# Performance work log

Measured on AMD Instinct MI355X. Metric: run time of the kernel, lower is better.

## Reference

```python
import jax, jax.numpy as jnp
import numpy as np
import math

B, T, EMB, HEAD = 4, 4096, 768, 64


def setup_inputs() -> dict:
    key = jax.random.key(0)
    kx, kk, kq, kv = jax.random.split(key, 4)
    s = 1.0 / math.sqrt(EMB)  # roughly torch Linear init scale
    return {
        "x": jax.random.normal(kx, (B, T, EMB), dtype=jnp.float32),
        "Wk": jax.random.normal(kk, (EMB, HEAD), dtype=jnp.float32) * s,
        "Wq": jax.random.normal(kq, (EMB, HEAD), dtype=jnp.float32) * s,
        "Wv": jax.random.normal(kv, (EMB, HEAD), dtype=jnp.float32) * s,
    }


def reference(x, Wk, Wq, Wv):
    # x: (B, T, EMB); projections are bias-free Linear layers
    k = x @ Wk  # (B, T, HEAD)
    q = x @ Wq
    v = x @ Wv
    Tcur = x.shape[1]
    scale = 1.0 / math.sqrt(k.shape[-1])
    # (B, Tq, Tk) score matrix, causal masked
    wei = jnp.einsum("bqh,bkh->bqk", q, k) * scale
    causal = jnp.tril(jnp.ones((Tcur, Tcur), dtype=bool))
    wei = jnp.where(causal, wei, -jnp.inf)
    attn = jax.nn.softmax(wei, axis=-1)  # dropout p=0.0 (eval)
    return jnp.einsum("bqk,bkh->bqh", attn, v)  # (B, T, HEAD)
```

## Files before the change

### kernel.cpp

```cpp
#include <hip/hip_runtime.h>
#include <hip/hip_bf16.h>

#define NB 4
#define NT 4096
#define NE 768
#define NH 64

using bf16 = __hip_bfloat16;
typedef __attribute__((ext_vector_type(8))) short bf16x8;
typedef __attribute__((ext_vector_type(4))) float f32x4;
typedef __attribute__((ext_vector_type(16))) float f32x16;
typedef __attribute__((ext_vector_type(4))) unsigned int u32x4;

#define QSCALE 0.18033688011112042f

__device__ inline short f2bfs(float f) {
  bf16 h = __float2bfloat16(f);
  return __builtin_bit_cast(short, h);
}
__device__ inline unsigned pack_bf2(float a, float b) {
  unsigned short ua = __builtin_bit_cast(unsigned short, __float2bfloat16(a));
  unsigned short ub = __builtin_bit_cast(unsigned short, __float2bfloat16(b));
  return ((unsigned)ub << 16) | ua;
}

#define GLOAD_LDS16(gsrc, ldst)                                        \
  __builtin_amdgcn_global_load_lds(                                    \
      (const __attribute__((address_space(1))) void*)(gsrc),           \
      (__attribute__((address_space(3))) void*)(ldst), 16, 0, 0)

__global__ __launch_bounds__(256) void k_wt(const float* __restrict__ Wk,
                                            const float* __restrict__ Wq,
                                            const float* __restrict__ Wv,
                                            bf16* __restrict__ Wt2) {
  __shared__ float xl[32][65];
  const int m = blockIdx.x / 24;
  const int ks = blockIdx.x % 24;
  const int tid = threadIdx.x;
  const float* W = (m == 0) ? Wk : ((m == 1) ? Wq : Wv);
  const float scale = (m == 1) ? QSCALE : 1.0f;
  const int e0 = ks * 32;
#pragma unroll
  for (int i = 0; i < 8; ++i) {
    const int lin = i * 256 + tid;
    xl[lin >> 6][lin & 63] = W[(size_t)(e0 + (lin >> 6)) * NH + (lin & 63)];
  }
  __syncthreads();
  const int lane = tid & 63, w = tid >> 6;
  const int cbg = m * 4 + w;
  bf16x8 t;
#pragma unroll
  for (int j = 0; j < 8; ++j)
    t[j] = f2bfs(xl[((lane >> 4) << 3) + j][w * 16 + (lane & 15)] * scale);
  *reinterpret_cast<bf16x8*>(Wt2 + (((size_t)cbg * 24 + ks) * 64 + lane) * 8) = t;
}

__global__ __launch_bounds__(256) void k_proj(const float* __restrict__ x,
                                              const bf16* __restrict__ Wt2,
                                              bf16* __restrict__ Q,
                                              bf16* __restrict__ K,
                                              bf16* __restrict__ Vt) {
  __shared__ __align__(16) bf16 xl[16][768];
  const int tid = threadIdx.x;
  const int wave = tid >> 6, lane = tid & 63;
  const int lr = lane & 15, lk = lane >> 4;
  const int row0 = blockIdx.x * 16;

#pragma unroll
  for (int j = 0; j < 6; ++j) {
    const int e = (j * 256 + tid) * 8;
    const int row = e / 768;
    const int col = e - row * 768;
    const int chunk = col >> 3;
    const int sch = (chunk & ~7) | ((chunk ^ row) & 7);
    const float* xp = x + (size_t)(row0 + row) * NE + col;
    float4 a0 = *reinterpret_cast<const float4*>(xp);
    float4 a1 = *reinterpret_cast<const float4*>(xp + 4);
    bf16x8 af;
    af[0] = f2bfs(a0.x); af[1] = f2bfs(a0.y); af[2] = f2bfs(a0.z); af[3] = f2bfs(a0.w);
    af[4] = f2bfs(a1.x); af[5] = f2bfs(a1.y); af[6] = f2bfs(a1.z); af[7] = f2bfs(a1.w);
    *reinterpret_cast<bf16x8*>((char*)xl + row * 1536 + sch * 16) = af;
  }
  __syncthreads();

  f32x4 acc[3];
#pragma unroll
  for (int cb = 0; cb < 3; ++cb)
#pragma unroll
    for (int r = 0; r < 4; ++r) acc[cb][r] = 0.f;

#pragma unroll 4
  for (int ks = 0; ks < 24; ++ks) {
    const int chunk = ks * 4 + lk;
    const int sch = (chunk & ~7) | ((chunk ^ lr) & 7);
    bf16x8 af = *reinterpret_cast<const bf16x8*>((const char*)xl + lr * 1536 + sch * 16);
#pragma unroll
    for (int cb = 0; cb < 3; ++cb) {
      bf16x8 bfr = *reinterpret_cast<const bf16x8*>(
          Wt2 + (((size_t)(wave * 3 + cb) * 24 + ks) * 64 + lane) * 8);
      acc[cb] = __builtin_amdgcn_mfma_f32_16x16x32_bf16(af, bfr, acc[cb], 0, 0, 0);
    }
  }

  const int trow = row0 + lk * 4;
#pragma unroll
  for (int cb = 0; cb < 3; ++cb) {
    const int hh0 = (wave * 3 + cb) * 16;
    const int m = hh0 >> 6;
    const int h = (hh0 & 63) + lr;
    if (m == 0) {
#pragma unroll
      for (int r = 0; r < 4; ++r)
        K[(size_t)(trow + r) * NH + h] = __float2bfloat16(acc[cb][r]);
    } else if (m == 1) {
#pragma unroll
      for (int r = 0; r < 4; ++r)
        Q[(size_t)(trow + r) * NH + h] = __float2bfloat16(acc[cb][r]);
    } else {
      const int bb = trow >> 12;
      const int t = trow & (NT - 1);
      ushort4 pk;
      pk.x = (unsigned short)f2bfs(acc[cb][0]);
      pk.y = (unsigned short)f2bfs(acc[cb][1]);
      pk.z = (unsigned short)f2bfs(acc[cb][2]);
      pk.w = (unsigned short)f2bfs(acc[cb][3]);
      *reinterpret_cast<ushort4*>(Vt + (size_t)(bb * NH + h) * NT + t) = pk;
    }
  }
}

__device__ inline void stage_kv(const bf16* Kb, const bf16* Vb, int k0,
                                bf16* Kl, bf16* Vl, int wave, int lane) {
  const int rsub = lane >> 3, ch = lane & 7;
#pragma unroll
  for (int j = 0; j < 2; ++j) {
    const int br = j * 32 + wave * 8;
    const int row = br + rsub;
    const int sch = ch ^ (row & 7);
    GLOAD_LDS16(Kb + (size_t)(k0 + row) * NH + sch * 8, Kl + br * 64);
    GLOAD_LDS16(Vb + (size_t)row * NT + k0 + sch * 8, Vl + br * 64);
  }
}

__global__ __launch_bounds__(256) void k_attn_part(const bf16* __restrict__ Q,
                                                   const bf16* __restrict__ K,
                                                   const bf16* __restrict__ Vt,
                                                   float* __restrict__ part_o,
                                                   float* __restrict__ part_ml,
                                                   int CH, int MAXC) {
  __shared__ __align__(16) bf16 Kl[2][64][64];
  __shared__ __align__(16) bf16 Vl[2][64][64];
  const int tid = threadIdx.x;
  const int wave = tid >> 6, lane = tid & 63;
  const int l31 = lane & 31, hi5 = lane >> 5;
  const int gid = blockIdx.x;
  const int c = gid % MAXC;
  const int srs = (gid / MAXC) & 31;
  const int b = gid / (MAXC * 32);
  const int s = 31 - srs;
  const int ntiles = 2 * s + 2;
  const int nch = (ntiles + CH - 1) / CH;
  if (c >= nch) return;
  const int kt0 = c * CH;
  const int kt1 = min(kt0 + CH, ntiles);
  const int qblk = s * 128;
  const int qrow = 8 * wave + (l31 & 7) + 32 * (l31 >> 3);
  const int qcol = qblk + qrow;

  const bf16* Qb = Q + (size_t)(b * NT + qcol) * NH;
  const bf16* Kb = K + (size_t)b * NT * NH;
  const bf16* Vb = Vt + (size_t)b * NH * NT;

  bf16x8 qf[4];
#pragma unroll
  for (int ks = 0; ks < 4; ++ks)
    qf[ks] = *reinterpret_cast<const bf16x8*>(Qb + ks * 16 + hi5 * 8);

  f32x16 o[2];
#pragma unroll
  for (int hb = 0; hb < 2; ++hb)
#pragma unroll
    for (int r = 0; r < 16; ++r) o[hb][r] = 0.f;
  float m = -1e30f, lsum = 0.f;

  stage_kv(Kb, Vb, kt0 * 64, &Kl[0][0][0], &Vl[0][0][0], wave, lane);

  for (int kt = kt0; kt < kt1; ++kt) {
    const int buf = (kt - kt0) & 1;
    __syncthreads();
    if (kt + 1 < kt1)
      stage_kv(Kb, Vb, (kt + 1) * 64, &Kl[buf ^ 1][0][0], &Vl[buf ^ 1][0][0], wave, lane);
    const int k0 = kt * 64;
    const bf16* Klb = &Kl[buf][0][0];
    const bf16* Vlb = &Vl[buf][0][0];

    f32x16 sa[2];
#pragma unroll
    for (int kb = 0; kb < 2; ++kb) {
#pragma unroll
      for (int r = 0; r < 16; ++r) sa[kb][r] = 0.f;
      __builtin_amdgcn_s_setprio(1);
#pragma unroll
      for (int ks = 0; ks < 4; ++ks) {
        const int row = l31 + 32 * kb;
        const int sch = (hi5 + 2 * ks) ^ (row & 7);
        bf16x8 kf = *reinterpret_cast<const bf16x8*>(Klb + row * 64 + sch * 8);
        sa[kb] = __builtin_amdgcn_mfma_f32_32x32x16_bf16(kf, qf[ks], sa[kb], 0, 0, 0);
      }
      __builtin_amdgcn_s_setprio(0);
    }
    if (kt >= 2 * s) {
#pragma unroll
      for (int kb = 0; kb < 2; ++kb)
#pragma unroll
        for (int r = 0; r < 16; ++r) {
          const int kg = k0 + (r & 3) + 8 * (r >> 2) + 4 * hi5 + 32 * kb;
          if (kg > qcol) sa[kb][r] = -1e30f;
        }
    }
    float pm = sa[0][0];
#pragma unroll
    for (int r = 1; r < 16; ++r) pm = fmaxf(pm, sa[0][r]);
#pragma unroll
    for (int r = 0; r < 16; ++r) pm = fmaxf(pm, sa[1][r]);
    pm = fmaxf(pm, __shfl_xor(pm, 32));
    if (!__all(pm - m <= 6.f)) {
      const float mn = fmaxf(m, pm);
      const float alpha = exp2f(m - mn);
      lsum *= alpha;
#pragma unroll
      for (int hb = 0; hb < 2; ++hb)
#pragma unroll
        for (int r = 0; r < 16; ++r) o[hb][r] *= alpha;
      m = mn;
    }
    float rs = 0.f;
#pragma unroll
    for (int kb = 0; kb < 2; ++kb)
#pragma unroll
      for (int r = 0; r < 16; ++r) {
        const float p = exp2f(sa[kb][r] - m);
        sa[kb][r] = p;
        rs += p;
      }
    rs += __shfl_xor(rs, 32);
    lsum += rs;
    unsigned pk[2][4][2];
#pragma unroll
    for (int kb = 0; kb < 2; ++kb)
#pragma unroll
      for (int q4 = 0; q4 < 4; ++q4)
#pragma unroll
        for (int p = 0; p < 2; ++p)
          pk[kb][q4][p] = pack_bf2(sa[kb][4 * q4 + 2 * p], sa[kb][4 * q4 + 2 * p + 1]);
#pragma unroll
    for (int kb16 = 0; kb16 < 4; ++kb16) {
      const int kb32 = kb16 >> 1;
      const int q4a = 2 * (kb16 & 1);
      const unsigned X0 = pk[kb32][q4a][0], X1 = pk[kb32][q4a][1];
      const unsigned Y0 = pk[kb32][q4a + 1][0], Y1 = pk[kb32][q4a + 1][1];
      const unsigned pX0 = __shfl_xor((int)X0, 32), pX1 = __shfl_xor((int)X1, 32);
      const unsigned pY0 = __shfl_xor((int)Y0, 32), pY1 = __shfl_xor((int)Y1, 32);
      u32x4 pw;
      pw[0] = hi5 ? pY0 : X0;
      pw[1] = hi5 ? pY1 : X1;
      pw[2] = hi5 ? Y0 : pX0;
      pw[3] = hi5 ? Y1 : pX1;
      const bf16x8 pf = __builtin_bit_cast(bf16x8, pw);
      __builtin_amdgcn_s_setprio(1);
#pragma unroll
      for (int hb = 0; hb < 2; ++hb) {
        const int row = l31 + 32 * hb;
        const int sch = (hi5 + 2 * kb16) ^ (row & 7);
        bf16x8 vf = *reinterpret_cast<const bf16x8*>(Vlb + row * 64 + sch * 8);
        o[hb] = __builtin_amdgcn_mfma_f32_32x32x16_bf16(vf, pf, o[hb], 0, 0, 0);
      }
      __builtin_amdgcn_s_setprio(0);
    }
  }

  const size_t idx = (size_t)(b * 32 + s) * MAXC + c;
  float* po = part_o + idx * (128 * 64);
#pragma unroll
  for (int hb = 0; hb < 2; ++hb)
#pragma unroll
    for (int q4 = 0; q4 < 4; ++q4) {
      const int h0 = 32 * hb + 8 * q4 + 4 * hi5;
      float4 v;
      v.x = o[hb][4 * q4 + 0];
      v.y = o[hb][4 * q4 + 1];
      v.z = o[hb][4 * q4 + 2];
      v.w = o[hb][4 * q4 + 3];
      *reinterpret_cast<float4*>(po + (size_t)qrow * 64 + h0) = v;
    }
  if (hi5 == 0) {
    float* pml = part_ml + idx * 256;
    pml[qrow] = m;
    pml[128 + qrow] = lsum;
  }
}

__global__ __launch_bounds__(256) void k_attn_comb(const float* __restrict__ part_o,
                                                   const float* __restrict__ part_ml,
                                                   float* __restrict__ out,
                                                   int CH, int MAXC) {
  const int gid = blockIdx.x;
  const int s = gid & 31;
  const int b = gid >> 5;
  const int row = threadIdx.x >> 1;
  const int half = threadIdx.x & 1;
  const int ntiles = 2 * s + 2;
  const int nc = (ntiles + CH - 1) / CH;
  const size_t base = (size_t)(b * 32 + s) * MAXC;

  float M = -1e30f;
  for (int c = 0; c < nc; ++c)
    M = fmaxf(M, part_ml[(base + c) * 256 + row]);
  float L = 0.f;
  float4 a[8];
#pragma unroll
  for (int k = 0; k < 8; ++k) a[k] = float4{0, 0, 0, 0};
  for (int c = 0; c < nc; ++c) {
    const float mc = part_ml[(base + c) * 256 + row];
    const float lc = part_ml[(base + c) * 256 + 128 + row];
    const float sc = exp2f(mc - M);
    L += lc * sc;
    const float4* op = reinterpret_cast<const float4*>(
        part_o + (base + c) * (128 * 64) + (size_t)row * 64 + half * 32);
#pragma unroll
    for (int k = 0; k < 8; ++k) {
      const float4 v = op[k];
      a[k].x += v.x * sc; a[k].y += v.y * sc;
      a[k].z += v.z * sc; a[k].w += v.w * sc;
    }
  }
  const float inv = 1.f / L;
  float4* outp = reinterpret_cast<float4*>(
      out + (size_t)(b * NT + s * 128 + row) * NH + half * 32);
#pragma unroll
  for (int k = 0; k < 8; ++k) {
    a[k].x *= inv; a[k].y *= inv; a[k].z *= inv; a[k].w *= inv;
    outp[k] = a[k];
  }
}

extern "C" void kernel_launch(void* const* d_in, const int* in_sizes, int n_in,
                              void* d_out, int out_size, void* d_ws, size_t ws_size,
                              hipStream_t stream) {
  const float* x  = (const float*)d_in[0];
  const float* Wk = (const float*)d_in[1];
  const float* Wq = (const float*)d_in[2];
  const float* Wv = (const float*)d_in[3];
  float* out = (float*)d_out;

  char* ws = (char*)d_ws;
  const size_t sz_wt  = (size_t)3 * NH * NE * sizeof(bf16);
  const size_t sz_qkv = (size_t)NB * NT * NH * sizeof(bf16);
  const size_t off_q  = (sz_wt + 255) & ~size_t(255);
  const size_t off_k  = off_q + sz_qkv;
  const size_t off_vt = off_k + sz_qkv;
  const size_t off_pp = off_vt + sz_qkv;

  const size_t per_chunk = (size_t)(128 * 64 + 256) * sizeof(float);
  int CH = 64, MAXC = 1;
  const int opts_ch[3]   = {6, 8, 16};
  const int opts_maxc[3] = {11, 8, 4};
  for (int i = 0; i < 3; ++i) {
    const size_t need = off_pp + (size_t)NB * 32 * opts_maxc[i] * per_chunk;
    if (ws_size >= need) { CH = opts_ch[i]; MAXC = opts_maxc[i]; break; }
  }
  const size_t n_idx = (size_t)NB * 32 * MAXC;
  const size_t off_po = off_pp;
  const size_t off_ml = off_po + n_idx * (128 * 64) * sizeof(float);

  bf16* Wt2 = (bf16*)(ws);
  bf16* Qw  = (bf16*)(ws + off_q);
  bf16* Kw  = (bf16*)(ws + off_k);
  bf16* Vtw = (bf16*)(ws + off_vt);
  float* part_o  = (float*)(ws + off_po);
  float* part_ml = (float*)(ws + off_ml);

  hipLaunchKernelGGL(k_wt, dim3(3 * 24), dim3(256), 0, stream, Wk, Wq, Wv, Wt2);
  hipLaunchKernelGGL(k_proj, dim3(NB * NT / 16), dim3(256), 0, stream,
                     x, Wt2, Qw, Kw, Vtw);
  hipLaunchKernelGGL(k_attn_part, dim3(NB * 32 * MAXC), dim3(256), 0, stream,
                     Qw, Kw, Vtw, part_o, part_ml, CH, MAXC);
  hipLaunchKernelGGL(k_attn_comb, dim3(NB * 32), dim3(256), 0, stream,
                     part_o, part_ml, out, CH, MAXC);
}
```

Baseline: 157.3 us.

## Software-pipeline QK^T ahead of softmax/PV, bf16 partials, wider projection and combine

The attention split kernel now triple-buffers K and double-buffers V, computing the next tile's QK^T scores before the current tile's softmax and PV MFMAs so that matrix work overlaps the exp/reduction phase. Partial outputs are stored as bf16 instead of fp32, which halves partial-buffer traffic but adds rounding error before the combine. The projection kernel processes 32 rows per block, reusing each weight fragment for two MFMAs. The combine kernel launches eight times more blocks, each handling fewer columns per thread. Register pressure rises from the extra score accumulators held across the pipeline.

```diff
diff --git a/kernel.cpp b/kernel.cpp
--- a/kernel.cpp
+++ b/kernel.cpp
@@ -17,6 +17,10 @@
 __device__ inline short f2bfs(float f) {
   bf16 h = __float2bfloat16(f);
   return __builtin_bit_cast(short, h);
+}
+__device__ inline float bfs2f(unsigned short u) {
+  unsigned v = ((unsigned)u) << 16;
+  return __builtin_bit_cast(float, v);
 }
 __device__ inline unsigned pack_bf2(float a, float b) {
   unsigned short ua = __builtin_bit_cast(unsigned short, __float2bfloat16(a));
@@ -60,14 +64,14 @@
                                               bf16* __restrict__ Q,
                                               bf16* __restrict__ K,
                                               bf16* __restrict__ Vt) {
-  __shared__ __align__(16) bf16 xl[16][768];
+  __shared__ __align__(16) bf16 xl[32][768];
   const int tid = threadIdx.x;
   const int wave = tid >> 6, lane = tid & 63;
   const int lr = lane & 15, lk = lane >> 4;
-  const int row0 = blockIdx.x * 16;
-
-#pragma unroll
-  for (int j = 0; j < 6; ++j) {
+  const int row0 = blockIdx.x * 32;
+
+#pragma unroll
+  for (int j = 0; j < 12; ++j) {
     const int e = (j * 256 + tid) * 8;
     const int row = e / 768;
     const int col = e - row * 768;
@@ -83,72 +87,182 @@
   }
   __syncthreads();
 
-  f32x4 acc[3];
+  f32x4 acc0[3], acc1[3];
 #pragma unroll
   for (int cb = 0; cb < 3; ++cb)
 #pragma unroll
-    for (int r = 0; r < 4; ++r) acc[cb][r] = 0.f;
+    for (int r = 0; r < 4; ++r) { acc0[cb][r] = 0.f; acc1[cb][r] = 0.f; }
 
 #pragma unroll 4
   for (int ks = 0; ks < 24; ++ks) {
     const int chunk = ks * 4 + lk;
     const int sch = (chunk & ~7) | ((chunk ^ lr) & 7);
-    bf16x8 af = *reinterpret_cast<const bf16x8*>((const char*)xl + lr * 1536 + sch * 16);
+    bf16x8 af0 = *reinterpret_cast<const bf16x8*>((const char*)xl + lr * 1536 + sch * 16);
+    bf16x8 af1 = *reinterpret_cast<const bf16x8*>((const char*)xl + (16 + lr) * 1536 + sch * 16);
 #pragma unroll
     for (int cb = 0; cb < 3; ++cb) {
       bf16x8 bfr = *reinterpret_cast<const bf16x8*>(
           Wt2 + (((size_t)(wave * 3 + cb) * 24 + ks) * 64 + lane) * 8);
-      acc[cb] = __builtin_amdgcn_mfma_f32_16x16x32_bf16(af, bfr, acc[cb], 0, 0, 0);
+      acc0[cb] = __builtin_amdgcn_mfma_f32_16x16x32_bf16(af0, bfr, acc0[cb], 0, 0, 0);
+      acc1[cb] = __builtin_amdgcn_mfma_f32_16x16x32_bf16(af1, bfr, acc1[cb], 0, 0, 0);
     }
   }
 
-  const int trow = row0 + lk * 4;
-#pragma unroll
-  for (int cb = 0; cb < 3; ++cb) {
-    const int hh0 = (wave * 3 + cb) * 16;
-    const int m = hh0 >> 6;
-    const int h = (hh0 & 63) + lr;
-    if (m == 0) {
-#pragma unroll
-      for (int r = 0; r < 4; ++r)
-        K[(size_t)(trow + r) * NH + h] = __float2bfloat16(acc[cb][r]);
-    } else if (m == 1) {
-#pragma unroll
-      for (int r = 0; r < 4; ++r)
-        Q[(size_t)(trow + r) * NH + h] = __float2bfloat16(acc[cb][r]);
-    } else {
-      const int bb = trow >> 12;
-      const int t = trow & (NT - 1);
-      ushort4 pk;
-      pk.x = (unsigned short)f2bfs(acc[cb][0]);
-      pk.y = (unsigned short)f2bfs(acc[cb][1]);
-      pk.z = (unsigned short)f2bfs(acc[cb][2]);
-      pk.w = (unsigned short)f2bfs(acc[cb][3]);
-      *reinterpret_cast<ushort4*>(Vt + (size_t)(bb * NH + h) * NT + t) = pk;
+#pragma unroll
+  for (int st = 0; st < 2; ++st) {
+    const int trow = row0 + st * 16 + lk * 4;
+#pragma unroll
+    for (int cb = 0; cb < 3; ++cb) {
+      const f32x4 a = st ? acc1[cb] : acc0[cb];
+      const int hh0 = (wave * 3 + cb) * 16;
+      const int m = hh0 >> 6;
+      const int h = (hh0 & 63) + lr;
+      if (m == 0) {
+#pragma unroll
+        for (int r = 0; r < 4; ++r)
+          K[(size_t)(trow + r) * NH + h] = __float2bfloat16(a[r]);
+      } else if (m == 1) {
+#pragma unroll
+        for (int r = 0; r < 4; ++r)
+          Q[(size_t)(trow + r) * NH + h] = __float2bfloat16(a[r]);
+      } else {
+        const int bb = trow >> 12;
+        const int t = trow & (NT - 1);
+        ushort4 pk;
+        pk.x = (unsigned short)f2bfs(a[0]);
+        pk.y = (unsigned short)f2bfs(a[1]);
+        pk.z = (unsigned short)f2bfs(a[2]);
+        pk.w = (unsigned short)f2bfs(a[3]);
+        *reinterpret_cast<ushort4*>(Vt + (size_t)(bb * NH + h) * NT + t) = pk;
+      }
     }
   }
 }
 
-__device__ inline void stage_kv(const bf16* Kb, const bf16* Vb, int k0,
-                                bf16* Kl, bf16* Vl, int wave, int lane) {
+__device__ inline void stage_k(const bf16* Kb, int k0, bf16* Kd, int wave, int lane) {
   const int rsub = lane >> 3, ch = lane & 7;
 #pragma unroll
   for (int j = 0; j < 2; ++j) {
     const int br = j * 32 + wave * 8;
     const int row = br + rsub;
     const int sch = ch ^ (row & 7);
-    GLOAD_LDS16(Kb + (size_t)(k0 + row) * NH + sch * 8, Kl + br * 64);
-    GLOAD_LDS16(Vb + (size_t)row * NT + k0 + sch * 8, Vl + br * 64);
-  }
-}
+    GLOAD_LDS16(Kb + (size_t)(k0 + row) * NH + sch * 8, Kd + br * 64);
+  }
+}
+__device__ inline void stage_v(const bf16* Vb, int k0, bf16* Vd, int wave, int lane) {
+  const int rsub = lane >> 3, ch = lane & 7;
+#pragma unroll
+  for (int j = 0; j < 2; ++j) {
+    const int br = j * 32 + wave * 8;
+    const int row = br + rsub;
+    const int sch = ch ^ (row & 7);
+    GLOAD_LDS16(Vb + (size_t)row * NT + k0 + sch * 8, Vd + br * 64);
+  }
+}
+
+#define QK_TILE(SA, KBUF, KT)                                                 \
+  {                                                                           \
+    const bf16* kbp_ = (KBUF);                                                \
+    _Pragma("unroll")                                                         \
+    for (int kb = 0; kb < 2; ++kb) {                                          \
+      _Pragma("unroll") for (int r = 0; r < 16; ++r) SA[kb][r] = 0.f;         \
+      __builtin_amdgcn_s_setprio(1);                                          \
+      _Pragma("unroll")                                                       \
+      for (int ks = 0; ks < 4; ++ks) {                                        \
+        const int row_ = l31 + 32 * kb;                                       \
+        const int sch_ = (hi5 + 2 * ks) ^ (row_ & 7);                         \
+        bf16x8 kf_ = *reinterpret_cast<const bf16x8*>(kbp_ + row_ * 64 + sch_ * 8); \
+        SA[kb] = __builtin_amdgcn_mfma_f32_32x32x16_bf16(kf_, qf[ks], SA[kb], 0, 0, 0); \
+      }                                                                       \
+      __builtin_amdgcn_s_setprio(0);                                          \
+    }                                                                         \
+    if ((KT) >= 2 * s) {                                                      \
+      _Pragma("unroll")                                                       \
+      for (int kb = 0; kb < 2; ++kb)                                          \
+        _Pragma("unroll") for (int r = 0; r < 16; ++r) {                      \
+          const int kg_ = (KT) * 64 + (r & 3) + 8 * (r >> 2) + 4 * hi5 + 32 * kb; \
+          if (kg_ > qcol) SA[kb][r] = -1e30f;                                 \
+        }                                                                     \
+    }                                                                         \
+  }
+
+#define TILE_BODY(SC, SN, I)                                                  \
+  {                                                                           \
+    __syncthreads();                                                          \
+    if ((I) + 2 < n) stage_k(Kb, (kt0 + (I) + 2) * 64, &Kl[((I) + 2) % 3][0][0], wave, lane); \
+    if ((I) + 1 < n) {                                                        \
+      stage_v(Vb, (kt0 + (I) + 1) * 64, &Vl[((I) + 1) & 1][0][0], wave, lane); \
+      QK_TILE(SN, &Kl[((I) + 1) % 3][0][0], kt0 + (I) + 1);                   \
+    }                                                                         \
+                               \
+    float t0_[8];                                                             \
+    _Pragma("unroll")                                                         \
+    for (int r = 0; r < 8; ++r)                                               \
+      t0_[r] = fmaxf(fmaxf(SC[0][r], SC[0][r + 8]), fmaxf(SC[1][r], SC[1][r + 8])); \
+    float pm = fmaxf(fmaxf(fmaxf(t0_[0], t0_[1]), fmaxf(t0_[2], t0_[3])),     \
+                     fmaxf(fmaxf(t0_[4], t0_[5]), fmaxf(t0_[6], t0_[7])));    \
+    pm = fmaxf(pm, __shfl_xor(pm, 32));                                       \
+    if (!__all(pm - m <= 6.f)) {                                              \
+      const float mn = fmaxf(m, pm);                                          \
+      const float alpha = exp2f(m - mn);                                      \
+      lsum *= alpha;                                                          \
+      _Pragma("unroll")                                                       \
+      for (int hb = 0; hb < 2; ++hb)                                          \
+        _Pragma("unroll") for (int r = 0; r < 16; ++r) o[hb][r] *= alpha;     \
+      m = mn;                                                                 \
+    }                                                                         \
+    float rs0 = 0.f, rs1 = 0.f, rs2 = 0.f, rs3 = 0.f;                         \
+    _Pragma("unroll")                                                         \
+    for (int kb = 0; kb < 2; ++kb)                                            \
+      _Pragma("unroll") for (int r = 0; r < 16; r += 4) {                     \
+        SC[kb][r] = exp2f(SC[kb][r] - m); rs0 += SC[kb][r];                   \
+        SC[kb][r + 1] = exp2f(SC[kb][r + 1] - m); rs1 += SC[kb][r + 1];       \
+        SC[kb][r + 2] = exp2f(SC[kb][r + 2] - m); rs2 += SC[kb][r + 2];       \
+        SC[kb][r + 3] = exp2f(SC[kb][r + 3] - m); rs3 += SC[kb][r + 3];       \
+      }                                                                       \
+    float rs = (rs0 + rs1) + (rs2 + rs3);                                     \
+    rs += __shfl_xor(rs, 32);                                                 \
+    lsum += rs;                                                               \
+    unsigned pk[2][4][2];                                                     \
+    _Pragma("unroll")                                                         \
+    for (int kb = 0; kb < 2; ++kb)                                            \
+      _Pragma("unroll") for (int q4 = 0; q4 < 4; ++q4)                        \
+        _Pragma("unroll") for (int p = 0; p < 2; ++p)                         \
+          pk[kb][q4][p] = pack_bf2(SC[kb][4 * q4 + 2 * p], SC[kb][4 * q4 + 2 * p + 1]); \
+    const bf16* Vlb_ = &Vl[(I) & 1][0][0];                                    \
+    _Pragma("unroll")                                                         \
+    for (int kb16 = 0; kb16 < 4; ++kb16) {                                    \
+      const int kb32 = kb16 >> 1;                                             \
+      const int q4a = 2 * (kb16 & 1);                                         \
+      const unsigned X0 = pk[kb32][q4a][0], X1 = pk[kb32][q4a][1];            \
+      const unsigned Y0 = pk[kb32][q4a + 1][0], Y1 = pk[kb32][q4a + 1][1];    \
+      const unsigned pX0 = __shfl_xor((int)X0, 32), pX1 = __shfl_xor((int)X1, 32); \
+      const unsigned pY0 = __shfl_xor((int)Y0, 32), pY1 = __shfl_xor((int)Y1, 32); \
+      u32x4 pw;                                                               \
+      pw[0] = hi5 ? pY0 : X0;                                                 \
+      pw[1] = hi5 ? pY1 : X1;                                                 \
+      pw[2] = hi5 ? Y0 : pX0;                                                 \
+      pw[3] = hi5 ? Y1 : pX1;                                                 \
+      const bf16x8 pf = __builtin_bit_cast(bf16x8, pw);                       \
+      __builtin_amdgcn_s_setprio(1);                                          \
+      _Pragma("unroll")                                                       \
+      for (int hb = 0; hb < 2; ++hb) {                                        \
+        const int row_ = l31 + 32 * hb;                                       \
+        const int sch_ = (hi5 + 2 * kb16) ^ (row_ & 7);                       \
+        bf16x8 vf = *reinterpret_cast<const bf16x8*>(Vlb_ + row_ * 64 + sch_ * 8); \
+        o[hb] = __builtin_amdgcn_mfma_f32_32x32x16_bf16(vf, pf, o[hb], 0, 0, 0); \
+      }                                                                       \
+      __builtin_amdgcn_s_setprio(0);                                          \
+    }                                                                         \
+  }
 
 __global__ __launch_bounds__(256) void k_attn_part(const bf16* __restrict__ Q,
                                                    const bf16* __restrict__ K,
                                                    const bf16* __restrict__ Vt,
-                                                   float* __restrict__ part_o,
+                                                   bf16* __restrict__ part_o,
                                                    float* __restrict__ part_ml,
                                                    int CH, int MAXC) {
-  __shared__ __align__(16) bf16 Kl[2][64][64];
+  __shared__ __align__(16) bf16 Kl[3][64][64];
   __shared__ __align__(16) bf16 Vl[2][64][64];
   const int tid = threadIdx.x;
   const int wave = tid >> 6, lane = tid & 63;
@@ -162,7 +276,7 @@
   const int nch = (ntiles + CH - 1) / CH;
   if (c >= nch) return;
   const int kt0 = c * CH;
-  const int kt1 = min(kt0 + CH, ntiles);
+  const int n = min(CH, ntiles - kt0);
   const int qblk = s * 128;
   const int qrow = 8 * wave + (l31 & 7) + 32 * (l31 >> 3);
   const int qcol = qblk + qrow;
@@ -183,115 +297,32 @@
     for (int r = 0; r < 16; ++r) o[hb][r] = 0.f;
   float m = -1e30f, lsum = 0.f;
 
-  stage_kv(Kb, Vb, kt0 * 64, &Kl[0][0][0], &Vl[0][0][0], wave, lane);
-
-  for (int kt = kt0; kt < kt1; ++kt) {
-    const int buf = (kt - kt0) & 1;
-    __syncthreads();
-    if (kt + 1 < kt1)
-      stage_kv(Kb, Vb, (kt + 1) * 64, &Kl[buf ^ 1][0][0], &Vl[buf ^ 1][0][0], wave, lane);
-    const int k0 = kt * 64;
-    const bf16* Klb = &Kl[buf][0][0];
-    const bf16* Vlb = &Vl[buf][0][0];
-
-    f32x16 sa[2];
-#pragma unroll
-    for (int kb = 0; kb < 2; ++kb) {
-#pragma unroll
-      for (int r = 0; r < 16; ++r) sa[kb][r] = 0.f;
-      __builtin_amdgcn_s_setprio(1);
-#pragma unroll
-      for (int ks = 0; ks < 4; ++ks) {
-        const int row = l31 + 32 * kb;
-        const int sch = (hi5 + 2 * ks) ^ (row & 7);
-        bf16x8 kf = *reinterpret_cast<const bf16x8*>(Klb + row * 64 + sch * 8);
-        sa[kb] = __builtin_amdgcn_mfma_f32_32x32x16_bf16(kf, qf[ks], sa[kb], 0, 0, 0);
-      }
-      __builtin_amdgcn_s_setprio(0);
-    }
-    if (kt >= 2 * s) {
-#pragma unroll
-      for (int kb = 0; kb < 2; ++kb)
-#pragma unroll
-        for (int r = 0; r < 16; ++r) {
-          const int kg = k0 + (r & 3) + 8 * (r >> 2) + 4 * hi5 + 32 * kb;
-          if (kg > qcol) sa[kb][r] = -1e30f;
-        }
-    }
-    float pm = sa[0][0];
-#pragma unroll
-    for (int r = 1; r < 16; ++r) pm = fmaxf(pm, sa[0][r]);
-#pragma unroll
-    for (int r = 0; r < 16; ++r) pm = fmaxf(pm, sa[1][r]);
-    pm = fmaxf(pm, __shfl_xor(pm, 32));
-    if (!__all(pm - m <= 6.f)) {
-      const float mn = fmaxf(m, pm);
-      const float alpha = exp2f(m - mn);
-      lsum *= alpha;
-#pragma unroll
-      for (int hb = 0; hb < 2; ++hb)
-#pragma unroll
-        for (int r = 0; r < 16; ++r) o[hb][r] *= alpha;
-      m = mn;
-    }
-    float rs = 0.f;
-#pragma unroll
-    for (int kb = 0; kb < 2; ++kb)
-#pragma unroll
-      for (int r = 0; r < 16; ++r) {
-        const float p = exp2f(sa[kb][r] - m);
-        sa[kb][r] = p;
-        rs += p;
-      }
-    rs += __shfl_xor(rs, 32);
-    lsum += rs;
-    unsigned pk[2][4][2];
-#pragma unroll
-    for (int kb = 0; kb < 2; ++kb)
-#pragma unroll
-      for (int q4 = 0; q4 < 4; ++q4)
-#pragma unroll
-        for (int p = 0; p < 2; ++p)
-          pk[kb][q4][p] = pack_bf2(sa[kb][4 * q4 + 2 * p], sa[kb][4 * q4 + 2 * p + 1]);
-#pragma unroll
-    for (int kb16 = 0; kb16 < 4; ++kb16) {
-      const int kb32 = kb16 >> 1;
-      const int q4a = 2 * (kb16 & 1);
-      const unsigned X0 = pk[kb32][q4a][0], X1 = pk[kb32][q4a][1];
-      const unsigned Y0 = pk[kb32][q4a + 1][0], Y1 = pk[kb32][q4a + 1][1];
-      const unsigned pX0 = __shfl_xor((int)X0, 32), pX1 = __shfl_xor((int)X1, 32);
-      const unsigned pY0 = __shfl_xor((int)Y0, 32), pY1 = __shfl_xor((int)Y1, 32);
-      u32x4 pw;
-      pw[0] = hi5 ? pY0 : X0;
-      pw[1] = hi5 ? pY1 : X1;
-      pw[2] = hi5 ? Y0 : pX0;
-      pw[3] = hi5 ? Y1 : pX1;
-      const bf16x8 pf = __builtin_bit_cast(bf16x8, pw);
-      __builtin_amdgcn_s_setprio(1);
-#pragma unroll
-      for (int hb = 0; hb < 2; ++hb) {
-        const int row = l31 + 32 * hb;
-        const int sch = (hi5 + 2 * kb16) ^ (row & 7);
-        bf16x8 vf = *reinterpret_cast<const bf16x8*>(Vlb + row * 64 + sch * 8);
-        o[hb] = __builtin_amdgcn_mfma_f32_32x32x16_bf16(vf, pf, o[hb], 0, 0, 0);
-      }
-      __builtin_amdgcn_s_setprio(0);
-    }
+  stage_k(Kb, kt0 * 64, &Kl[0][0][0], wave, lane);
+  stage_v(Vb, kt0 * 64, &Vl[0][0][0], wave, lane);
+  __syncthreads();
+  if (n > 1) stage_k(Kb, (kt0 + 1) * 64, &Kl[1][0][0], wave, lane);
+  f32x16 saA[2], saB[2];
+  QK_TILE(saA, &Kl[0][0][0], kt0);
+
+  int i = 0;
+  for (;;) {
+    TILE_BODY(saA, saB, i); if (++i >= n) break;
+    TILE_BODY(saB, saA, i); if (++i >= n) break;
   }
 
   const size_t idx = (size_t)(b * 32 + s) * MAXC + c;
-  float* po = part_o + idx * (128 * 64);
+  bf16* po = part_o + idx * (128 * 64);
 #pragma unroll
   for (int hb = 0; hb < 2; ++hb)
 #pragma unroll
     for (int q4 = 0; q4 < 4; ++q4) {
       const int h0 = 32 * hb + 8 * q4 + 4 * hi5;
-      float4 v;
-      v.x = o[hb][4 * q4 + 0];
-      v.y = o[hb][4 * q4 + 1];
-      v.z = o[hb][4 * q4 + 2];
-      v.w = o[hb][4 * q4 + 3];
-      *reinterpret_cast<float4*>(po + (size_t)qrow * 64 + h0) = v;
+      ushort4 pk4;
+      pk4.x = (unsigned short)f2bfs(o[hb][4 * q4 + 0]);
+      pk4.y = (unsigned short)f2bfs(o[hb][4 * q4 + 1]);
+      pk4.z = (unsigned short)f2bfs(o[hb][4 * q4 + 2]);
+      pk4.w = (unsigned short)f2bfs(o[hb][4 * q4 + 3]);
+      *reinterpret_cast<ushort4*>(po + (size_t)qrow * 64 + h0) = pk4;
     }
   if (hi5 == 0) {
     float* pml = part_ml + idx * 256;
@@ -300,15 +331,16 @@
   }
 }
 
-__global__ __launch_bounds__(256) void k_attn_comb(const float* __restrict__ part_o,
+__global__ __launch_bounds__(256) void k_attn_comb(const bf16* __restrict__ part_o,
                                                    const float* __restrict__ part_ml,
                                                    float* __restrict__ out,
                                                    int CH, int MAXC) {
   const int gid = blockIdx.x;
-  const int s = gid & 31;
-  const int b = gid >> 5;
-  const int row = threadIdx.x >> 1;
-  const int half = threadIdx.x & 1;
+  const int rg = gid & 7;
+  const int s = (gid >> 3) & 31;
+  const int b = gid >> 8;
+  const int row = rg * 16 + (threadIdx.x >> 4);
+  const int cq = threadIdx.x & 15;
   const int ntiles = 2 * s + 2;
   const int nc = (ntiles + CH - 1) / CH;
   const size_t base = (size_t)(b * 32 + s) * MAXC;
@@ -316,32 +348,24 @@
   float M = -1e30f;
   for (int c = 0; c < nc; ++c)
     M = fmaxf(M, part_ml[(base + c) * 256 + row]);
-  float L = 0.f;
-  float4 a[8];
-#pragma unroll
-  for (int k = 0; k < 8; ++k) a[k] = float4{0, 0, 0, 0};
+  float L = 0.f, a0 = 0.f, a1 = 0.f, a2 = 0.f, a3 = 0.f;
   for (int c = 0; c < nc; ++c) {
     const float mc = part_ml[(base + c) * 256 + row];
     const float lc = part_ml[(base + c) * 256 + 128 + row];
     const float sc = exp2f(mc - M);
     L += lc * sc;
-    const float4* op = reinterpret_cast<const float4*>(
-        part_o + (base + c) * (128 * 64) + (size_t)row * 64 + half * 32);
-#pragma unroll
-    for (int k = 0; k < 8; ++k) {
-      const float4 v = op[k];
-      a[k].x += v.x * sc; a[k].y += v.y * sc;
-      a[k].z += v.z * sc; a[k].w += v.w * sc;
-    }
+    ushort4 v = *reinterpret_cast<const ushort4*>(
+        part_o + (base + c) * (128 * 64) + (size_t)row * 64 + cq * 4);
+    a0 += bfs2f(v.x) * sc;
+    a1 += bfs2f(v.y) * sc;
+    a2 += bfs2f(v.z) * sc;
+    a3 += bfs2f(v.w) * sc;
   }
   const float inv = 1.f / L;
-  float4* outp = reinterpret_cast<float4*>(
-      out + (size_t)(b * NT + s * 128 + row) * NH + half * 32);
-#pragma unroll
-  for (int k = 0; k < 8; ++k) {
-    a[k].x *= inv; a[k].y *= inv; a[k].z *= inv; a[k].w *= inv;
-    outp[k] = a[k];
-  }
+  float4 ov;
+  ov.x = a0 * inv; ov.y = a1 * inv; ov.z = a2 * inv; ov.w = a3 * inv;
+  *reinterpret_cast<float4*>(
+      out + (size_t)(b * NT + s * 128 + row) * NH + cq * 4) = ov;
 }
 
 extern "C" void kernel_launch(void* const* d_in, const int* in_sizes, int n_in,
@@ -361,7 +385,7 @@
   const size_t off_vt = off_k + sz_qkv;
   const size_t off_pp = off_vt + sz_qkv;
 
-  const size_t per_chunk = (size_t)(128 * 64 + 256) * sizeof(float);
+  const size_t per_chunk = (size_t)128 * 64 * sizeof(bf16) + 256 * sizeof(float);
   int CH = 64, MAXC = 1;
   const int opts_ch[3]   = {6, 8, 16};
   const int opts_maxc[3] = {11, 8, 4};
@@ -371,20 +395,20 @@
   }
   const size_t n_idx = (size_t)NB * 32 * MAXC;
   const size_t off_po = off_pp;
-  const size_t off_ml = off_po + n_idx * (128 * 64) * sizeof(float);
+  const size_t off_ml = off_po + n_idx * (size_t)(128 * 64) * sizeof(bf16);
 
   bf16* Wt2 = (bf16*)(ws);
   bf16* Qw  = (bf16*)(ws + off_q);
   bf16* Kw  = (bf16*)(ws + off_k);
   bf16* Vtw = (bf16*)(ws + off_vt);
-  float* part_o  = (float*)(ws + off_po);
+  bf16* part_o   = (bf16*)(ws + off_po);
   float* part_ml = (float*)(ws + off_ml);
 
   hipLaunchKernelGGL(k_wt, dim3(3 * 24), dim3(256), 0, stream, Wk, Wq, Wv, Wt2);
-  hipLaunchKernelGGL(k_proj, dim3(NB * NT / 16), dim3(256), 0, stream,
+  hipLaunchKernelGGL(k_proj, dim3(NB * NT / 32), dim3(256), 0, stream,
                      x, Wt2, Qw, Kw, Vtw);
   hipLaunchKernelGGL(k_attn_part, dim3(NB * 32 * MAXC), dim3(256), 0, stream,
                      Qw, Kw, Vtw, part_o, part_ml, CH, MAXC);
-  hipLaunchKernelGGL(k_attn_comb, dim3(NB * 32), dim3(256), 0, stream,
+  hipLaunchKernelGGL(k_attn_comb, dim3(NB * 32 * 8), dim3(256), 0, stream,
                      part_o, part_ml, out, CH, MAXC);
 }
```

Result: slower. 183.5 us (+16.7%).
